# Optimization experiments

Hardware: AMD Instinct MI355X
Metric: run time of the kernel (lower is better)

Reference implementation:

```python
import jax, jax.numpy as jnp
import numpy as np

N_NODES = 50000
N_EDGES = 800000
IN_CH = 128
HID = 32
HEADS = 4
LATENT = 64
NEG_SLOPE = 0.2  # PyG GATConv default


def setup_inputs() -> dict:
    key = jax.random.key(0)
    ks = jax.random.split(key, 12)
    HC = HID * HEADS
    inp = {
        "x": jax.random.normal(ks[0], (N_NODES, IN_CH), dtype=jnp.float32),
        "edge_index": jax.random.randint(ks[1], (2, N_EDGES), 0, N_NODES, dtype=jnp.int64),
        # GATConv params
        "W_gat": jax.random.normal(ks[2], (IN_CH, HC), dtype=jnp.float32) / np.sqrt(IN_CH),
        "b_gat": jnp.zeros((HC,), dtype=jnp.float32),
        "att_src": jax.random.normal(ks[3], (HEADS, HID), dtype=jnp.float32) / np.sqrt(HID),
        "att_dst": jax.random.normal(ks[4], (HEADS, HID), dtype=jnp.float32) / np.sqrt(HID),
        # encoder / decoder / output linears
        "W_enc": jax.random.normal(ks[5], (HC, LATENT), dtype=jnp.float32) / np.sqrt(HC),
        "b_enc": jnp.zeros((LATENT,), dtype=jnp.float32),
        "W_dec": jax.random.normal(ks[6], (LATENT, HC), dtype=jnp.float32) / np.sqrt(LATENT),
        "b_dec": jnp.zeros((HC,), dtype=jnp.float32),
        "W_out": jax.random.normal(ks[7], (HC, IN_CH), dtype=jnp.float32) / np.sqrt(HC),
        "b_out": jnp.zeros((IN_CH,), dtype=jnp.float32),
    }
    return inp


def reference(x, edge_index, W_gat, b_gat, att_src, att_dst,
              W_enc, b_enc, W_dec, b_dec, W_out, b_out):
    N = x.shape[0]
    H, C = att_src.shape
    # PyG GATConv adds self-loops by default
    loops = jnp.arange(N, dtype=edge_index.dtype)
    src = jnp.concatenate([edge_index[0], loops])  # message sources (x_j)
    dst = jnp.concatenate([edge_index[1], loops])  # aggregation targets (x_i)

    h = (x @ W_gat).reshape(N, H, C)               # [N,H,C]
    a_src = jnp.einsum('nhc,hc->nh', h, att_src)   # [N,H]
    a_dst = jnp.einsum('nhc,hc->nh', h, att_dst)   # [N,H]

    e = jax.nn.leaky_relu(a_src[src] + a_dst[dst], NEG_SLOPE)  # [E,H]
    # segment softmax over destination nodes (numerically stable)
    e_max = jax.ops.segment_max(e, dst, num_segments=N)
    e_exp = jnp.exp(e - e_max[dst])
    denom = jax.ops.segment_sum(e_exp, dst, num_segments=N)
    alpha = e_exp / (denom[dst] + 1e-16)           # [E,H]

    msg = h[src] * alpha[:, :, None]               # [E,H,C]
    agg = jax.ops.segment_sum(msg, dst, num_segments=N)  # [N,H,C]
    gat_out = agg.reshape(N, H * C) + b_gat        # concat heads + bias

    x1 = jax.nn.elu(gat_out)
    encoded = x1 @ W_enc + b_enc
    decoded = encoded @ W_dec + b_dec
    x2 = jax.nn.elu(decoded)
    return x2 @ W_out + b_out
```

## Files before the change

kernel.cpp:

```cpp
#include <hip/hip_runtime.h>
#include <hip/hip_bf16.h>

#define N_NODES 50000
#define N_EDGES 800000
#define BM 64
#define NBUCK 196
#define CAP 8192
#define CHUNK 2048
#define NCHUNK ((N_EDGES + CHUNK - 1) / CHUNK)
#define SUBCAP 32
#define DCAP 5120
#define SWZ_BLOCKS 192
#define SWZ_G 32768
#define GBLK ((N_NODES + BM - 1) / BM)
#define SXP 136
#define SEP 72
#define SMEM_BYTES (64 * SXP * 2 + 64 * 132 * 4)

typedef _Float16 half4v __attribute__((ext_vector_type(4)));
typedef _Float16 half8 __attribute__((ext_vector_type(8)));
typedef float    float4v __attribute__((ext_vector_type(4)));

__device__ __forceinline__ float elu_f(float v) {
    return (v > 0.f) ? v : (__expf(v) - 1.f);
}

__device__ __forceinline__ unsigned f2bf2(float a, float b) {
    unsigned ua = __float_as_uint(a), ub = __float_as_uint(b);
    ua = (ua + 0x7FFFu + ((ua >> 16) & 1u)) >> 16;
    ub = (ub + 0x7FFFu + ((ub >> 16) & 1u)) >> 16;
    return ua | (ub << 16);
}
__device__ __forceinline__ float2 bf2f2(unsigned u) {
    float2 f;
    f.x = __uint_as_float(u << 16);
    f.y = __uint_as_float(u & 0xFFFF0000u);
    return f;
}

__global__ __launch_bounds__(256) void k_pre_bucket(const void* __restrict__ e_raw,
        const float* __restrict__ We, const float* __restrict__ Wd,
        const float* __restrict__ Wo, const float* __restrict__ Wg,
        _Float16* __restrict__ swz, uint2* __restrict__ ebuck2,
        int* __restrict__ cnt) {
    const int b = blockIdx.x;
    const int tid = threadIdx.x;
    if (b >= SWZ_BLOCKS) {
        __shared__ int lh[256];
        __shared__ int isl;
        const int c = b - SWZ_BLOCKS;
        const int base = c * CHUNK;
        const long long* e64 = (const long long*)e_raw;
        const int* e32 = (const int*)e_raw;
        if (tid == 0) {
            const unsigned* er = (const unsigned*)e_raw;
            int nz = 0;
            for (int j = 0; j < 64; j++) nz |= (er[2 * (base + j) + 1] != 0u);
            isl = nz ? 0 : 1;
        }
        lh[tid] = 0;
        __syncthreads();
        const int is64 = isl;
#pragma unroll 4
        for (int j = 0; j < CHUNK / 256; j++) {
            int e = base + j * 256 + tid;
            if (e < N_EDGES) {
                int sN, d;
                if (is64) { sN = (int)e64[e]; d = (int)e64[N_EDGES + e]; }
                else      { sN = e32[e];      d = e32[N_EDGES + e]; }
                int bb = d >> 8;
                int pos = atomicAdd(&lh[bb], 1);
                if (pos < SUBCAP) {
                    uint2 pr; pr.x = (unsigned)sN; pr.y = (unsigned)d;
                    ebuck2[((size_t)bb * NCHUNK + c) * SUBCAP + pos] = pr;
                }
            }
        }
        __syncthreads();
        int v = lh[tid]; if (v > SUBCAP) v = SUBCAP;
        cnt[c * 256 + tid] = v;
        return;
    }
    int t = b * 256 + tid;
    const float* W; int base, N;
    if (t < 8192)       { W = We; base = 0;     N = 64;  }
    else if (t < 16384) { W = Wd; base = 8192;  N = 128; }
    else if (t < 32768) { W = Wo; base = 16384; N = 128; }
    else                { W = Wg; base = SWZ_G; N = 128; }
    int loc = t - base;
    int nnt = N >> 4;
    int frag = loc >> 9, r = loc & 511, lane = r >> 3, j = r & 7;
    int kc = frag / nnt, nt = frag - kc * nnt;
    int k = kc * 32 + ((lane >> 4) << 3) + j;
    int n = nt * 16 + (lane & 15);
    swz[t] = (_Float16)W[k * N + n];
}

__global__ __launch_bounds__(256) void k_lin_bfill(
        const float* __restrict__ x, const _Float16* __restrict__ swz,
        const float* __restrict__ att_s, const float* __restrict__ att_d,
        unsigned* __restrict__ h_bf, float* __restrict__ a_src,
        float* __restrict__ a_dst,
        const uint2* __restrict__ ebuck2, const int* __restrict__ cnt,
        int2* __restrict__ nodeoff, int* __restrict__ csr_src) {
    __shared__ __align__(16) char smem[SMEM_BYTES];
    const int tid = threadIdx.x;

    if (blockIdx.x < NBUCK) {
        uint2* dense = (uint2*)smem;
        int*   coff  = (int*)(smem + 40960);
        int*   sc    = (int*)(smem + 42528);
        int*   lh    = (int*)(smem + 43552);
        int*   lexc  = (int*)(smem + 44576);
        int*   lcur  = (int*)(smem + 45600);
        const int bkt = blockIdx.x;
        const int lo = bkt * CAP;
        const int n0 = bkt << 8;

        int v0 = cnt[tid * 256 + bkt];
        sc[tid] = v0;
        __syncthreads();
        for (int o = 1; o < 256; o <<= 1) {
            int u = (tid >= o) ? sc[tid - o] : 0;
            __syncthreads();
            sc[tid] += u;
            __syncthreads();
        }
        coff[tid] = sc[tid] - v0;
        int total0 = sc[255];
        __syncthreads();
        int c2 = tid + 256;
        int v1 = (c2 < NCHUNK) ? cnt[c2 * 256 + bkt] : 0;
        sc[tid] = v1;
        __syncthreads();
        for (int o = 1; o < 256; o <<= 1) {
            int u = (tid >= o) ? sc[tid - o] : 0;
            __syncthreads();
            sc[tid] += u;
            __syncthreads();
        }
        if (c2 < NCHUNK) coff[c2] = total0 + sc[tid] - v1;
        int cntb = total0 + sc[255];
        if (cntb > DCAP) cntb = DCAP;
        if (tid == 0) coff[NCHUNK] = cntb;
        __syncthreads();

        {
            int cg = tid >> 3, j = tid & 7;
            for (int c = cg; c < NCHUNK; c += 32) {
                int off = coff[c];
                int n = coff[c + 1] - off;
                const uint2* src = &ebuck2[((size_t)bkt * NCHUNK + c) * SUBCAP];
                for (int e = j; e < n; e += 8)
                    if (off + e < DCAP) dense[off + e] = src[e];
            }
        }
        __syncthreads();

        lh[tid] = 0;
        lcur[tid] = 0;
        __syncthreads();
        for (int i = tid; i < cntb; i += 256)
            atomicAdd(&lh[dense[i].y & 255], 1);
        __syncthreads();

        int v = lh[tid];
        int p = (v + 7) & ~7;
        lexc[tid] = p;
        __syncthreads();
        for (int o = 1; o < 256; o <<= 1) {
            int u = (tid >= o) ? lexc[tid - o] : 0;
            __syncthreads();
            lexc[tid] += u;
            __syncthreads();
        }
        {
            int s = lexc[tid] - p;
            lexc[tid] = s;
            int node = n0 + tid;
            if (node < N_NODES) {
                int2 no;
                no.x = lo + s;
                int maxlen = CAP - s; if (maxlen < 0) maxlen = 0;
                no.y = p <= maxlen ? p : (maxlen & ~7);
                nodeoff[node] = no;
            }
        }
        __syncthreads();

        for (int i = tid; i < cntb; i += 256) {
            uint2 pr = dense[i];
            int li = (int)(pr.y & 255);
            int pos = atomicAdd(&lcur[li], 1);
            int dst = lexc[li] + pos;
            if (dst < CAP) csr_src[lo + dst] = (int)pr.x;
        }
        {
            int base2 = lexc[tid];
            for (int j = v; j < p && base2 + j < CAP; j++)
                csr_src[lo + base2 + j] = -1;
        }
        return;
    }

    _Float16* sx = (_Float16*)smem;
    float*    sh = (float*)(smem + 64 * SXP * 2);
    const int m0 = (blockIdx.x - NBUCK) * 64;

#pragma unroll
    for (int i = 0; i < 8; i++) {
        int idx = tid + i * 256;
        int r = idx >> 5, c4 = idx & 31;
        int row = m0 + r; if (row >= N_NODES) row = N_NODES - 1;
        float4 v = ((const float4*)(x + (size_t)row * 128))[c4];
        half4v h;
        h[0] = (_Float16)v.x; h[1] = (_Float16)v.y;
        h[2] = (_Float16)v.z; h[3] = (_Float16)v.w;
        *(half4v*)&sx[r * SXP + c4 * 4] = h;
    }
    __syncthreads();

    const int wave = tid >> 6, lane = tid & 63;
    const int lm = lane & 15, lq = lane >> 4;
    const int wrow = wave * 16;

    {
        float4v acc[8];
#pragma unroll
        for (int nt = 0; nt < 8; nt++) acc[nt] = (float4v){0.f, 0.f, 0.f, 0.f};
#pragma unroll
        for (int kc = 0; kc < 4; kc++) {
            half8 a = *(const half8*)&sx[(wrow + lm) * SXP + kc * 32 + lq * 8];
#pragma unroll
            for (int nt = 0; nt < 8; nt++) {
                half8 b = *(const half8*)&swz[SWZ_G + (kc * 8 + nt) * 512 + lane * 8];
                acc[nt] = __builtin_amdgcn_mfma_f32_16x16x32_f16(a, b, acc[nt], 0, 0, 0);
            }
        }
#pragma unroll
        for (int nt = 0; nt < 8; nt++)
#pragma unroll
            for (int r = 0; r < 4; r++)
                sh[(wrow + lq * 4 + r) * 132 + nt * 16 + lm] = acc[nt][r];
    }
    __syncthreads();

    const int c0 = (tid & 31) * 4;
    const int r0 = (tid >> 5) * 8;
    float4 as4 = *(const float4*)&att_s[c0];
    float4 ad4 = *(const float4*)&att_d[c0];
    const int head = c0 >> 5;

#pragma unroll
    for (int r = 0; r < 8; r++) {
        int row = m0 + r0 + r;
        bool ok = row < N_NODES;
        float4 hv = *(const float4*)&sh[(r0 + r) * 132 + c0];
        if (ok) {
            uint2 p;
            p.x = f2bf2(hv.x, hv.y);
            p.y = f2bf2(hv.z, hv.w);
            *(uint2*)&h_bf[(size_t)row * 64 + (c0 >> 1)] = p;
        }
        float vs = hv.x * as4.x + hv.y * as4.y + hv.z * as4.z + hv.w * as4.w;
        float vd = hv.x * ad4.x + hv.y * ad4.y + hv.z * ad4.z + hv.w * ad4.w;
#pragma unroll
        for (int o = 4; o >= 1; o >>= 1) {
            vs += __shfl_down(vs, o, 8);
            vd += __shfl_down(vd, o, 8);
        }
        if (ok && (tid & 7) == 0) {
            a_src[row * 4 + head] = vs;
            a_dst[row * 4 + head] = vd;
        }
    }
}

__global__ __launch_bounds__(256) void k_gather(const int2* __restrict__ nodeoff,
        const int* __restrict__ csr_src, const float* __restrict__ a_src,
        const float* __restrict__ a_dst, const unsigned* __restrict__ h_bf,
        const float* __restrict__ b_gat, _Float16* __restrict__ x1) {
    int d = blockIdx.x * 4 + (threadIdx.x >> 6);
    if (d >= N_NODES) return;
    const int lane = threadIdx.x & 63;
    const int eg = lane >> 4;
    const int lc = lane & 15;
    const int hd = lc >> 2;
    const uint4* hb = (const uint4*)h_bf;
    int2 nd = nodeoff[d];
    const int lo = nd.x, hi = nd.x + nd.y;

    const float adh = a_dst[(unsigned)(d * 4 + hd)];

    float den = 0.f;
    float c0 = 0.f, c1 = 0.f, c2 = 0.f, c3 = 0.f;
    float c4 = 0.f, c5 = 0.f, c6 = 0.f, c7 = 0.f;

    if (eg == 0) {
        float t = a_src[(unsigned)(d * 4 + hd)] + adh;
        t = t > 0.f ? t : 0.2f * t;
        float es = __expf(t);
        den = es;
        uint4 u = hb[(unsigned)d * 16 + lc];
        float2 p0 = bf2f2(u.x), p1 = bf2f2(u.y), p2 = bf2f2(u.z), p3 = bf2f2(u.w);
        c0 = p0.x * es; c1 = p0.y * es; c2 = p1.x * es; c3 = p1.y * es;
        c4 = p2.x * es; c5 = p2.y * es; c6 = p3.x * es; c7 = p3.y * es;
    }

    for (int base = lo; base < hi; base += 8) {
        int2 sv = *(const int2*)&csr_src[base + eg * 2];
        int sA = sv.x, sB = sv.y;
        unsigned gA = (unsigned)(sA < 0 ? d : sA);
        unsigned gB = (unsigned)(sB < 0 ? d : sB);
        uint4 uA = hb[gA * 16 + lc];
        uint4 uB = hb[gB * 16 + lc];
        float aA = a_src[gA * 4 + hd];
        float aB = a_src[gB * 4 + hd];

        float tA = aA + adh; tA = tA > 0.f ? tA : 0.2f * tA;
        float tB = aB + adh; tB = tB > 0.f ? tB : 0.2f * tB;
        float eA = sA < 0 ? 0.f : __expf(tA);
        float eB = sB < 0 ? 0.f : __expf(tB);
        den += eA + eB;

        float2 p0, p1, p2, p3;
        p0 = bf2f2(uA.x); p1 = bf2f2(uA.y); p2 = bf2f2(uA.z); p3 = bf2f2(uA.w);
        c0 = fmaf(p0.x, eA, c0); c1 = fmaf(p0.y, eA, c1);
        c2 = fmaf(p1.x, eA, c2); c3 = fmaf(p1.y, eA, c3);
        c4 = fmaf(p2.x, eA, c4); c5 = fmaf(p2.y, eA, c5);
        c6 = fmaf(p3.x, eA, c6); c7 = fmaf(p3.y, eA, c7);
        p0 = bf2f2(uB.x); p1 = bf2f2(uB.y); p2 = bf2f2(uB.z); p3 = bf2f2(uB.w);
        c0 = fmaf(p0.x, eB, c0); c1 = fmaf(p0.y, eB, c1);
        c2 = fmaf(p1.x, eB, c2); c3 = fmaf(p1.y, eB, c3);
        c4 = fmaf(p2.x, eB, c4); c5 = fmaf(p2.y, eB, c5);
        c6 = fmaf(p3.x, eB, c6); c7 = fmaf(p3.y, eB, c7);
    }

    den += __shfl_xor(den, 16);
    c0 += __shfl_xor(c0, 16); c1 += __shfl_xor(c1, 16);
    c2 += __shfl_xor(c2, 16); c3 += __shfl_xor(c3, 16);
    c4 += __shfl_xor(c4, 16); c5 += __shfl_xor(c5, 16);
    c6 += __shfl_xor(c6, 16); c7 += __shfl_xor(c7, 16);
    den += __shfl_xor(den, 32);
    c0 += __shfl_xor(c0, 32); c1 += __shfl_xor(c1, 32);
    c2 += __shfl_xor(c2, 32); c3 += __shfl_xor(c3, 32);
    c4 += __shfl_xor(c4, 32); c5 += __shfl_xor(c5, 32);
    c6 += __shfl_xor(c6, 32); c7 += __shfl_xor(c7, 32);

    if (lane < 16) {
        float inv = 1.f / (den + 1e-16f);
        float4 bg0 = ((const float4*)b_gat)[lc * 2];
        float4 bg1 = ((const float4*)b_gat)[lc * 2 + 1];
        half8 hv;
        hv[0] = (_Float16)elu_f(fmaf(c0, inv, bg0.x));
        hv[1] = (_Float16)elu_f(fmaf(c1, inv, bg0.y));
        hv[2] = (_Float16)elu_f(fmaf(c2, inv, bg0.z));
        hv[3] = (_Float16)elu_f(fmaf(c3, inv, bg0.w));
        hv[4] = (_Float16)elu_f(fmaf(c4, inv, bg1.x));
        hv[5] = (_Float16)elu_f(fmaf(c5, inv, bg1.y));
        hv[6] = (_Float16)elu_f(fmaf(c6, inv, bg1.z));
        hv[7] = (_Float16)elu_f(fmaf(c7, inv, bg1.w));
        *(half8*)&x1[(size_t)d * 128 + lc * 8] = hv;
    }
}

__global__ __launch_bounds__(256) void k_mlp(const _Float16* __restrict__ x1,
        const _Float16* __restrict__ swz, const float* __restrict__ b_enc,
        const float* __restrict__ b_dec, const float* __restrict__ b_out,
        float* __restrict__ out) {
    __shared__ _Float16 sx[64 * SXP];
    __shared__ _Float16 se[4 * 16 * SEP];
    const int tid = threadIdx.x;
    const int m0 = blockIdx.x * 64;

#pragma unroll
    for (int i = 0; i < 4; i++) {
        int idx = tid + i * 256;
        int r = idx >> 4, c = idx & 15;
        int row = m0 + r; if (row >= N_NODES) row = N_NODES - 1;
        uint4 v = ((const uint4*)(x1 + (size_t)row * 128))[c];
        *(uint4*)&sx[r * SXP + c * 8] = v;
    }
    __syncthreads();

    const int wave = tid >> 6, lane = tid & 63;
    const int lm = lane & 15, lq = lane >> 4;
    const int wrow = wave * 16;
    _Float16* eslab = &se[wave * 16 * SEP];

    {
        float4v acc[4];
#pragma unroll
        for (int nt = 0; nt < 4; nt++) acc[nt] = (float4v){0.f, 0.f, 0.f, 0.f};
#pragma unroll
        for (int kc = 0; kc < 4; kc++) {
            half8 a = *(const half8*)&sx[(wrow + lm) * SXP + kc * 32 + lq * 8];
#pragma unroll
            for (int nt = 0; nt < 4; nt++) {
                half8 b = *(const half8*)&swz[(kc * 4 + nt) * 512 + lane * 8];
                acc[nt] = __builtin_amdgcn_mfma_f32_16x16x32_f16(a, b, acc[nt], 0, 0, 0);
            }
        }
#pragma unroll
        for (int nt = 0; nt < 4; nt++) {
            float be = b_enc[nt * 16 + lm];
#pragma unroll
            for (int r = 0; r < 4; r++)
                eslab[(lq * 4 + r) * SEP + nt * 16 + lm] = (_Float16)(acc[nt][r] + be);
        }
    }

    {
        float4v acc[8];
#pragma unroll
        for (int nt = 0; nt < 8; nt++) acc[nt] = (float4v){0.f, 0.f, 0.f, 0.f};
#pragma unroll
        for (int kc = 0; kc < 2; kc++) {
            half8 a = *(const half8*)&eslab[lm * SEP + kc * 32 + lq * 8];
#pragma unroll
            for (int nt = 0; nt < 8; nt++) {
                half8 b = *(const half8*)&swz[8192 + (kc * 8 + nt) * 512 + lane * 8];
                acc[nt] = __builtin_amdgcn_mfma_f32_16x16x32_f16(a, b, acc[nt], 0, 0, 0);
            }
        }
#pragma unroll
        for (int nt = 0; nt < 8; nt++) {
            float bd = b_dec[nt * 16 + lm];
#pragma unroll
            for (int r = 0; r < 4; r++)
                sx[(wrow + lq * 4 + r) * SXP + nt * 16 + lm] =
                    (_Float16)elu_f(acc[nt][r] + bd);
        }
    }

    {
        float4v acc[8];
#pragma unroll
        for (int nt = 0; nt < 8; nt++) acc[nt] = (float4v){0.f, 0.f, 0.f, 0.f};
#pragma unroll
        for (int kc = 0; kc < 4; kc++) {
            half8 a = *(const half8*)&sx[(wrow + lm) * SXP + kc * 32 + lq * 8];
#pragma unroll
            for (int nt = 0; nt < 8; nt++) {
                half8 b = *(const half8*)&swz[16384 + (kc * 8 + nt) * 512 + lane * 8];
                acc[nt] = __builtin_amdgcn_mfma_f32_16x16x32_f16(a, b, acc[nt], 0, 0, 0);
            }
        }
#pragma unroll
        for (int nt = 0; nt < 8; nt++) {
            float bo = b_out[nt * 16 + lm];
#pragma unroll
            for (int r = 0; r < 4; r++) {
                int row = m0 + wrow + lq * 4 + r;
                if (row < N_NODES)
                    out[(size_t)row * 128 + nt * 16 + lm] = acc[nt][r] + bo;
            }
        }
    }
}

extern "C" void kernel_launch(void* const* d_in, const int* in_sizes, int n_in,
                              void* d_out, int out_size, void* d_ws, size_t ws_size,
                              hipStream_t stream) {
    const float* x       = (const float*)d_in[0];
    const void*  e_raw   = d_in[1];
    const float* W_gat   = (const float*)d_in[2];
    const float* b_gat   = (const float*)d_in[3];
    const float* att_src = (const float*)d_in[4];
    const float* att_dst = (const float*)d_in[5];
    const float* W_enc   = (const float*)d_in[6];
    const float* b_enc   = (const float*)d_in[7];
    const float* W_dec   = (const float*)d_in[8];
    const float* b_dec   = (const float*)d_in[9];
    const float* W_out   = (const float*)d_in[10];
    const float* b_out   = (const float*)d_in[11];
    float* out = (float*)d_out;

    float* ws      = (float*)d_ws;
    unsigned* h_bf = (unsigned*)ws;
    float* a_src   = ws + 6400000;
    float* a_dst   = a_src + 200000;
    float* agg     = a_dst + 200000;
    uint2* ebuck2  = (uint2*)agg;
    _Float16* x1   = (_Float16*)agg;
    int*   csr_src = (int*)(agg + 6400000);
    int*   cnt     = csr_src + NBUCK * CAP;
    int2*  nodeoff = (int2*)(cnt + NCHUNK * 256);
    _Float16* swz  = (_Float16*)(((uintptr_t)(nodeoff + 50000) + 15) & ~(uintptr_t)15);

    k_pre_bucket<<<SWZ_BLOCKS + NCHUNK, 256, 0, stream>>>(
        e_raw, W_enc, W_dec, W_out, W_gat, swz, ebuck2, cnt);

    k_lin_bfill<<<NBUCK + GBLK, 256, 0, stream>>>(
        x, swz, att_src, att_dst, h_bf, a_src, a_dst,
        ebuck2, cnt, nodeoff, csr_src);

    k_gather<<<(N_NODES + 3) / 4, 256, 0, stream>>>(
        nodeoff, csr_src, a_src, a_dst, h_bf, b_gat, x1);

    k_mlp<<<GBLK, 256, 0, stream>>>(x1, swz, b_enc, b_dec, b_out, out);
}
```

Measured before the change: 175.3 us.

## Fuse GAT gather with MLP chain in one 1024-thread block kernel

Merges the edge gather/softmax-aggregation kernel and the three-layer MFMA MLP kernel into one kernel. Each 1024-thread block gathers 64 destination nodes (4 per wave) straight into shared memory, then 16 waves split the MLP output columns. This removes the fp16 x1 round trip through global memory and one kernel launch. In exchange it adds block-wide barriers between stages, and the large blocks may lower occupancy and leave waves idle when node degrees are uneven.

```diff
diff --git a/kernel.cpp b/kernel.cpp
--- a/kernel.cpp
+++ b/kernel.cpp
@@ -276,184 +276,178 @@
     }
 }
 
-__global__ __launch_bounds__(256) void k_gather(const int2* __restrict__ nodeoff,
-        const int* __restrict__ csr_src, const float* __restrict__ a_src,
-        const float* __restrict__ a_dst, const unsigned* __restrict__ h_bf,
-        const float* __restrict__ b_gat, _Float16* __restrict__ x1) {
-    int d = blockIdx.x * 4 + (threadIdx.x >> 6);
-    if (d >= N_NODES) return;
-    const int lane = threadIdx.x & 63;
+__global__ __launch_bounds__(1024) void k_gather_mlp(
+        const int2* __restrict__ nodeoff, const int* __restrict__ csr_src,
+        const float* __restrict__ a_src, const float* __restrict__ a_dst,
+        const unsigned* __restrict__ h_bf, const float* __restrict__ b_gat,
+        const _Float16* __restrict__ swz, const float* __restrict__ b_enc,
+        const float* __restrict__ b_dec, const float* __restrict__ b_out,
+        float* __restrict__ out) {
+    __shared__ _Float16 sx[64 * SXP];
+    __shared__ _Float16 se[64 * SEP];
+    const int tid = threadIdx.x;
+    const int wave = tid >> 6, lane = tid & 63;
+    const int m0 = blockIdx.x * 64;
     const int eg = lane >> 4;
     const int lc = lane & 15;
     const int hd = lc >> 2;
     const uint4* hb = (const uint4*)h_bf;
-    int2 nd = nodeoff[d];
-    const int lo = nd.x, hi = nd.x + nd.y;
-
-    const float adh = a_dst[(unsigned)(d * 4 + hd)];
-
-    float den = 0.f;
-    float c0 = 0.f, c1 = 0.f, c2 = 0.f, c3 = 0.f;
-    float c4 = 0.f, c5 = 0.f, c6 = 0.f, c7 = 0.f;
-
-    if (eg == 0) {
-        float t = a_src[(unsigned)(d * 4 + hd)] + adh;
-        t = t > 0.f ? t : 0.2f * t;
-        float es = __expf(t);
-        den = es;
-        uint4 u = hb[(unsigned)d * 16 + lc];
-        float2 p0 = bf2f2(u.x), p1 = bf2f2(u.y), p2 = bf2f2(u.z), p3 = bf2f2(u.w);
-        c0 = p0.x * es; c1 = p0.y * es; c2 = p1.x * es; c3 = p1.y * es;
-        c4 = p2.x * es; c5 = p2.y * es; c6 = p3.x * es; c7 = p3.y * es;
-    }
-
-    for (int base = lo; base < hi; base += 8) {
-        int2 sv = *(const int2*)&csr_src[base + eg * 2];
-        int sA = sv.x, sB = sv.y;
-        unsigned gA = (unsigned)(sA < 0 ? d : sA);
-        unsigned gB = (unsigned)(sB < 0 ? d : sB);
-        uint4 uA = hb[gA * 16 + lc];
-        uint4 uB = hb[gB * 16 + lc];
-        float aA = a_src[gA * 4 + hd];
-        float aB = a_src[gB * 4 + hd];
-
-        float tA = aA + adh; tA = tA > 0.f ? tA : 0.2f * tA;
-        float tB = aB + adh; tB = tB > 0.f ? tB : 0.2f * tB;
-        float eA = sA < 0 ? 0.f : __expf(tA);
-        float eB = sB < 0 ? 0.f : __expf(tB);
-        den += eA + eB;
-
-        float2 p0, p1, p2, p3;
-        p0 = bf2f2(uA.x); p1 = bf2f2(uA.y); p2 = bf2f2(uA.z); p3 = bf2f2(uA.w);
-        c0 = fmaf(p0.x, eA, c0); c1 = fmaf(p0.y, eA, c1);
-        c2 = fmaf(p1.x, eA, c2); c3 = fmaf(p1.y, eA, c3);
-        c4 = fmaf(p2.x, eA, c4); c5 = fmaf(p2.y, eA, c5);
-        c6 = fmaf(p3.x, eA, c6); c7 = fmaf(p3.y, eA, c7);
-        p0 = bf2f2(uB.x); p1 = bf2f2(uB.y); p2 = bf2f2(uB.z); p3 = bf2f2(uB.w);
-        c0 = fmaf(p0.x, eB, c0); c1 = fmaf(p0.y, eB, c1);
-        c2 = fmaf(p1.x, eB, c2); c3 = fmaf(p1.y, eB, c3);
-        c4 = fmaf(p2.x, eB, c4); c5 = fmaf(p2.y, eB, c5);
-        c6 = fmaf(p3.x, eB, c6); c7 = fmaf(p3.y, eB, c7);
-    }
-
-    den += __shfl_xor(den, 16);
-    c0 += __shfl_xor(c0, 16); c1 += __shfl_xor(c1, 16);
-    c2 += __shfl_xor(c2, 16); c3 += __shfl_xor(c3, 16);
-    c4 += __shfl_xor(c4, 16); c5 += __shfl_xor(c5, 16);
-    c6 += __shfl_xor(c6, 16); c7 += __shfl_xor(c7, 16);
-    den += __shfl_xor(den, 32);
-    c0 += __shfl_xor(c0, 32); c1 += __shfl_xor(c1, 32);
-    c2 += __shfl_xor(c2, 32); c3 += __shfl_xor(c3, 32);
-    c4 += __shfl_xor(c4, 32); c5 += __shfl_xor(c5, 32);
-    c6 += __shfl_xor(c6, 32); c7 += __shfl_xor(c7, 32);
-
-    if (lane < 16) {
-        float inv = 1.f / (den + 1e-16f);
-        float4 bg0 = ((const float4*)b_gat)[lc * 2];
-        float4 bg1 = ((const float4*)b_gat)[lc * 2 + 1];
-        half8 hv;
-        hv[0] = (_Float16)elu_f(fmaf(c0, inv, bg0.x));
-        hv[1] = (_Float16)elu_f(fmaf(c1, inv, bg0.y));
-        hv[2] = (_Float16)elu_f(fmaf(c2, inv, bg0.z));
-        hv[3] = (_Float16)elu_f(fmaf(c3, inv, bg0.w));
-        hv[4] = (_Float16)elu_f(fmaf(c4, inv, bg1.x));
-        hv[5] = (_Float16)elu_f(fmaf(c5, inv, bg1.y));
-        hv[6] = (_Float16)elu_f(fmaf(c6, inv, bg1.z));
-        hv[7] = (_Float16)elu_f(fmaf(c7, inv, bg1.w));
-        *(half8*)&x1[(size_t)d * 128 + lc * 8] = hv;
-    }
-}
-
-__global__ __launch_bounds__(256) void k_mlp(const _Float16* __restrict__ x1,
-        const _Float16* __restrict__ swz, const float* __restrict__ b_enc,
-        const float* __restrict__ b_dec, const float* __restrict__ b_out,
-        float* __restrict__ out) {
-    __shared__ _Float16 sx[64 * SXP];
-    __shared__ _Float16 se[4 * 16 * SEP];
-    const int tid = threadIdx.x;
-    const int m0 = blockIdx.x * 64;
-
-#pragma unroll
-    for (int i = 0; i < 4; i++) {
-        int idx = tid + i * 256;
-        int r = idx >> 4, c = idx & 15;
-        int row = m0 + r; if (row >= N_NODES) row = N_NODES - 1;
-        uint4 v = ((const uint4*)(x1 + (size_t)row * 128))[c];
-        *(uint4*)&sx[r * SXP + c * 8] = v;
+    const float4 bg0 = ((const float4*)b_gat)[lc * 2];
+    const float4 bg1 = ((const float4*)b_gat)[lc * 2 + 1];
+
+    for (int k = 0; k < 4; k++) {
+        const int r = wave * 4 + k;
+        const int d = m0 + r;
+        if (d < N_NODES) {
+            int2 nd = nodeoff[d];
+            const int lo = nd.x, hi = nd.x + nd.y;
+            const float adh = a_dst[(unsigned)(d * 4 + hd)];
+
+            float den = 0.f;
+            float c0 = 0.f, c1 = 0.f, c2 = 0.f, c3 = 0.f;
+            float c4 = 0.f, c5 = 0.f, c6 = 0.f, c7 = 0.f;
+
+            if (eg == 0) {
+                float t = a_src[(unsigned)(d * 4 + hd)] + adh;
+                t = t > 0.f ? t : 0.2f * t;
+                float es = __expf(t);
+                den = es;
+                uint4 u = hb[(unsigned)d * 16 + lc];
+                float2 p0 = bf2f2(u.x), p1 = bf2f2(u.y),
+                       p2 = bf2f2(u.z), p3 = bf2f2(u.w);
+                c0 = p0.x * es; c1 = p0.y * es; c2 = p1.x * es; c3 = p1.y * es;
+                c4 = p2.x * es; c5 = p2.y * es; c6 = p3.x * es; c7 = p3.y * es;
+            }
+
+            for (int base = lo; base < hi; base += 8) {
+                int2 sv = *(const int2*)&csr_src[base + eg * 2];
+                int sA = sv.x, sB = sv.y;
+                unsigned gA = (unsigned)(sA < 0 ? d : sA);
+                unsigned gB = (unsigned)(sB < 0 ? d : sB);
+                uint4 uA = hb[gA * 16 + lc];
+                uint4 uB = hb[gB * 16 + lc];
+                float aA = a_src[gA * 4 + hd];
+                float aB = a_src[gB * 4 + hd];
+
+                float tA = aA + adh; tA = tA > 0.f ? tA : 0.2f * tA;
+                float tB = aB + adh; tB = tB > 0.f ? tB : 0.2f * tB;
+                float eA = sA < 0 ? 0.f : __expf(tA);
+                float eB = sB < 0 ? 0.f : __expf(tB);
+                den += eA + eB;
+
+                float2 p0, p1, p2, p3;
+                p0 = bf2f2(uA.x); p1 = bf2f2(uA.y);
+                p2 = bf2f2(uA.z); p3 = bf2f2(uA.w);
+                c0 = fmaf(p0.x, eA, c0); c1 = fmaf(p0.y, eA, c1);
+                c2 = fmaf(p1.x, eA, c2); c3 = fmaf(p1.y, eA, c3);
+                c4 = fmaf(p2.x, eA, c4); c5 = fmaf(p2.y, eA, c5);
+                c6 = fmaf(p3.x, eA, c6); c7 = fmaf(p3.y, eA, c7);
+                p0 = bf2f2(uB.x); p1 = bf2f2(uB.y);
+                p2 = bf2f2(uB.z); p3 = bf2f2(uB.w);
+                c0 = fmaf(p0.x, eB, c0); c1 = fmaf(p0.y, eB, c1);
+                c2 = fmaf(p1.x, eB, c2); c3 = fmaf(p1.y, eB, c3);
+                c4 = fmaf(p2.x, eB, c4); c5 = fmaf(p2.y, eB, c5);
+                c6 = fmaf(p3.x, eB, c6); c7 = fmaf(p3.y, eB, c7);
+            }
+
+            den += __shfl_xor(den, 16);
+            c0 += __shfl_xor(c0, 16); c1 += __shfl_xor(c1, 16);
+            c2 += __shfl_xor(c2, 16); c3 += __shfl_xor(c3, 16);
+            c4 += __shfl_xor(c4, 16); c5 += __shfl_xor(c5, 16);
+            c6 += __shfl_xor(c6, 16); c7 += __shfl_xor(c7, 16);
+            den += __shfl_xor(den, 32);
+            c0 += __shfl_xor(c0, 32); c1 += __shfl_xor(c1, 32);
+            c2 += __shfl_xor(c2, 32); c3 += __shfl_xor(c3, 32);
+            c4 += __shfl_xor(c4, 32); c5 += __shfl_xor(c5, 32);
+            c6 += __shfl_xor(c6, 32); c7 += __shfl_xor(c7, 32);
+
+            if (eg == 0) {
+                float inv = 1.f / (den + 1e-16f);
+                half8 hv;
+                hv[0] = (_Float16)elu_f(fmaf(c0, inv, bg0.x));
+                hv[1] = (_Float16)elu_f(fmaf(c1, inv, bg0.y));
+                hv[2] = (_Float16)elu_f(fmaf(c2, inv, bg0.z));
+                hv[3] = (_Float16)elu_f(fmaf(c3, inv, bg0.w));
+                hv[4] = (_Float16)elu_f(fmaf(c4, inv, bg1.x));
+                hv[5] = (_Float16)elu_f(fmaf(c5, inv, bg1.y));
+                hv[6] = (_Float16)elu_f(fmaf(c6, inv, bg1.z));
+                hv[7] = (_Float16)elu_f(fmaf(c7, inv, bg1.w));
+                *(half8*)&sx[r * SXP + lc * 8] = hv;
+            }
+        } else if (eg == 0) {
+            *(half8*)&sx[r * SXP + lc * 8] = (half8){0, 0, 0, 0, 0, 0, 0, 0};
+        }
     }
     __syncthreads();
 
-    const int wave = tid >> 6, lane = tid & 63;
     const int lm = lane & 15, lq = lane >> 4;
-    const int wrow = wave * 16;
-    _Float16* eslab = &se[wave * 16 * SEP];
+    const int wr = wave >> 2, wn = wave & 3;
+    const int wrow = wr * 16;
 
     {
-        float4v acc[4];
-#pragma unroll
-        for (int nt = 0; nt < 4; nt++) acc[nt] = (float4v){0.f, 0.f, 0.f, 0.f};
+        float4v acc = (float4v){0.f, 0.f, 0.f, 0.f};
 #pragma unroll
         for (int kc = 0; kc < 4; kc++) {
             half8 a = *(const half8*)&sx[(wrow + lm) * SXP + kc * 32 + lq * 8];
-#pragma unroll
-            for (int nt = 0; nt < 4; nt++) {
-                half8 b = *(const half8*)&swz[(kc * 4 + nt) * 512 + lane * 8];
-                acc[nt] = __builtin_amdgcn_mfma_f32_16x16x32_f16(a, b, acc[nt], 0, 0, 0);
-            }
-        }
-#pragma unroll
-        for (int nt = 0; nt < 4; nt++) {
-            float be = b_enc[nt * 16 + lm];
-#pragma unroll
-            for (int r = 0; r < 4; r++)
-                eslab[(lq * 4 + r) * SEP + nt * 16 + lm] = (_Float16)(acc[nt][r] + be);
-        }
-    }
+            half8 b = *(const half8*)&swz[(kc * 4 + wn) * 512 + lane * 8];
+            acc = __builtin_amdgcn_mfma_f32_16x16x32_f16(a, b, acc, 0, 0, 0);
+        }
+        float be = b_enc[wn * 16 + lm];
+#pragma unroll
+        for (int r = 0; r < 4; r++)
+            se[(wrow + lq * 4 + r) * SEP + wn * 16 + lm] = (_Float16)(acc[r] + be);
+    }
+    __syncthreads();
 
     {
-        float4v acc[8];
-#pragma unroll
-        for (int nt = 0; nt < 8; nt++) acc[nt] = (float4v){0.f, 0.f, 0.f, 0.f};
+        float4v acc[2];
+        acc[0] = (float4v){0.f, 0.f, 0.f, 0.f};
+        acc[1] = (float4v){0.f, 0.f, 0.f, 0.f};
 #pragma unroll
         for (int kc = 0; kc < 2; kc++) {
-            half8 a = *(const half8*)&eslab[lm * SEP + kc * 32 + lq * 8];
-#pragma unroll
-            for (int nt = 0; nt < 8; nt++) {
+            half8 a = *(const half8*)&se[(wrow + lm) * SEP + kc * 32 + lq * 8];
+#pragma unroll
+            for (int t = 0; t < 2; t++) {
+                int nt = wn * 2 + t;
                 half8 b = *(const half8*)&swz[8192 + (kc * 8 + nt) * 512 + lane * 8];
-                acc[nt] = __builtin_amdgcn_mfma_f32_16x16x32_f16(a, b, acc[nt], 0, 0, 0);
-            }
-        }
-#pragma unroll
-        for (int nt = 0; nt < 8; nt++) {
+                acc[t] = __builtin_amdgcn_mfma_f32_16x16x32_f16(a, b, acc[t], 0, 0, 0);
+            }
+        }
+#pragma unroll
+        for (int t = 0; t < 2; t++) {
+            int nt = wn * 2 + t;
             float bd = b_dec[nt * 16 + lm];
 #pragma unroll
             for (int r = 0; r < 4; r++)
                 sx[(wrow + lq * 4 + r) * SXP + nt * 16 + lm] =
-                    (_Float16)elu_f(acc[nt][r] + bd);
-        }
-    }
+                    (_Float16)elu_f(acc[t][r] + bd);
+        }
+    }
+    __syncthreads();
 
     {
-        float4v acc[8];
-#pragma unroll
-        for (int nt = 0; nt < 8; nt++) acc[nt] = (float4v){0.f, 0.f, 0.f, 0.f};
+        float4v acc[2];
+        acc[0] = (float4v){0.f, 0.f, 0.f, 0.f};
+        acc[1] = (float4v){0.f, 0.f, 0.f, 0.f};
 #pragma unroll
         for (int kc = 0; kc < 4; kc++) {
             half8 a = *(const half8*)&sx[(wrow + lm) * SXP + kc * 32 + lq * 8];
 #pragma unroll
-            for (int nt = 0; nt < 8; nt++) {
+            for (int t = 0; t < 2; t++) {
+                int nt = wn * 2 + t;
                 half8 b = *(const half8*)&swz[16384 + (kc * 8 + nt) * 512 + lane * 8];
-                acc[nt] = __builtin_amdgcn_mfma_f32_16x16x32_f16(a, b, acc[nt], 0, 0, 0);
-            }
-        }
-#pragma unroll
-        for (int nt = 0; nt < 8; nt++) {
+                acc[t] = __builtin_amdgcn_mfma_f32_16x16x32_f16(a, b, acc[t], 0, 0, 0);
+            }
+        }
+#pragma unroll
+        for (int t = 0; t < 2; t++) {
+            int nt = wn * 2 + t;
             float bo = b_out[nt * 16 + lm];
 #pragma unroll
             for (int r = 0; r < 4; r++) {
                 int row = m0 + wrow + lq * 4 + r;
                 if (row < N_NODES)
-                    out[(size_t)row * 128 + nt * 16 + lm] = acc[nt][r] + bo;
+                    out[(size_t)row * 128 + nt * 16 + lm] = acc[t][r] + bo;
             }
         }
     }
@@ -482,7 +476,6 @@
     float* a_dst   = a_src + 200000;
     float* agg     = a_dst + 200000;
     uint2* ebuck2  = (uint2*)agg;
-    _Float16* x1   = (_Float16*)agg;
     int*   csr_src = (int*)(agg + 6400000);
     int*   cnt     = csr_src + NBUCK * CAP;
     int2*  nodeoff = (int2*)(cnt + NCHUNK * 256);
@@ -495,8 +488,7 @@
         x, swz, att_src, att_dst, h_bf, a_src, a_dst,
         ebuck2, cnt, nodeoff, csr_src);
 
-    k_gather<<<(N_NODES + 3) / 4, 256, 0, stream>>>(
-        nodeoff, csr_src, a_src, a_dst, h_bf, b_gat, x1);
-
-    k_mlp<<<GBLK, 256, 0, stream>>>(x1, swz, b_enc, b_dec, b_out, out);
-}
+    k_gather_mlp<<<GBLK, 1024, 0, stream>>>(
+        nodeoff, csr_src, a_src, a_dst, h_bf, b_gat, swz,
+        b_enc, b_dec, b_out, out);
+}
```

New measurement: 176.0 us. No clear change (+0.4%).

## Split h into per-head planes and gather each head in a separate block set

Applied to the files above, without the earlier changes.

The bf16 projected features are stored as four head-major planes instead of interleaved rows. The gather kernel launches four times as many blocks, one set per head. Each wavefront processes 32 edges per iteration for a single head, using 4 lanes per 64-byte row. The aim is a smaller working set per head plane for better L2 hit rate and more parallelism on low-degree nodes. In exchange, each edge index and a_src value is re-read four times, and padded slots are now guarded with bounds checks.

```diff
diff --git a/kernel.cpp b/kernel.cpp
--- a/kernel.cpp
+++ b/kernel.cpp
@@ -16,6 +16,9 @@
 #define SXP 136
 #define SEP 72
 #define SMEM_BYTES (64 * SXP * 2 + 64 * 132 * 4)
+#define NQ 4
+#define NBPQ ((N_NODES + 3) / 4)
+#define HPLANE 800000
 
 typedef _Float16 half4v __attribute__((ext_vector_type(4)));
 typedef _Float16 half8 __attribute__((ext_vector_type(8)));
@@ -250,6 +253,8 @@
     float4 as4 = *(const float4*)&att_s[c0];
     float4 ad4 = *(const float4*)&att_d[c0];
     const int head = c0 >> 5;
+    const int pl = c0 >> 5;
+    const int ci = (c0 & 31) >> 1;
 
 #pragma unroll
     for (int r = 0; r < 8; r++) {
@@ -260,7 +265,7 @@
             uint2 p;
             p.x = f2bf2(hv.x, hv.y);
             p.y = f2bf2(hv.z, hv.w);
-            *(uint2*)&h_bf[(size_t)row * 64 + (c0 >> 1)] = p;
+            *(uint2*)&h_bf[(size_t)pl * HPLANE + (size_t)row * 16 + ci] = p;
         }
         float vs = hv.x * as4.x + hv.y * as4.y + hv.z * as4.z + hv.w * as4.w;
         float vd = hv.x * ad4.x + hv.y * ad4.y + hv.z * ad4.z + hv.w * ad4.w;
@@ -280,42 +285,46 @@
         const int* __restrict__ csr_src, const float* __restrict__ a_src,
         const float* __restrict__ a_dst, const unsigned* __restrict__ h_bf,
         const float* __restrict__ b_gat, _Float16* __restrict__ x1) {
-    int d = blockIdx.x * 4 + (threadIdx.x >> 6);
+    const int q  = blockIdx.x / NBPQ;
+    const int nb = blockIdx.x - q * NBPQ;
+    int d = nb * 4 + (threadIdx.x >> 6);
     if (d >= N_NODES) return;
     const int lane = threadIdx.x & 63;
-    const int eg = lane >> 4;
-    const int lc = lane & 15;
-    const int hd = lc >> 2;
-    const uint4* hb = (const uint4*)h_bf;
+    const int eg  = lane >> 2;
+    const int lc2 = lane & 3;
+    const uint4* hb = (const uint4*)(h_bf + (size_t)q * HPLANE);
     int2 nd = nodeoff[d];
     const int lo = nd.x, hi = nd.x + nd.y;
 
-    const float adh = a_dst[(unsigned)(d * 4 + hd)];
+    const float adh = a_dst[(unsigned)(d * 4 + q)];
 
     float den = 0.f;
     float c0 = 0.f, c1 = 0.f, c2 = 0.f, c3 = 0.f;
     float c4 = 0.f, c5 = 0.f, c6 = 0.f, c7 = 0.f;
 
     if (eg == 0) {
-        float t = a_src[(unsigned)(d * 4 + hd)] + adh;
+        float t = a_src[(unsigned)(d * 4 + q)] + adh;
         t = t > 0.f ? t : 0.2f * t;
         float es = __expf(t);
         den = es;
-        uint4 u = hb[(unsigned)d * 16 + lc];
+        uint4 u = hb[(unsigned)d * 4 + lc2];
         float2 p0 = bf2f2(u.x), p1 = bf2f2(u.y), p2 = bf2f2(u.z), p3 = bf2f2(u.w);
         c0 = p0.x * es; c1 = p0.y * es; c2 = p1.x * es; c3 = p1.y * es;
         c4 = p2.x * es; c5 = p2.y * es; c6 = p3.x * es; c7 = p3.y * es;
     }
 
-    for (int base = lo; base < hi; base += 8) {
-        int2 sv = *(const int2*)&csr_src[base + eg * 2];
-        int sA = sv.x, sB = sv.y;
+    for (int base = lo; base < hi; base += 32) {
+        int i0 = base + eg * 2;
+        int2 sv = *(const int2*)&csr_src[i0];
+        bool ok = i0 < hi;
+        int sA = ok ? sv.x : -1;
+        int sB = ok ? sv.y : -1;
         unsigned gA = (unsigned)(sA < 0 ? d : sA);
         unsigned gB = (unsigned)(sB < 0 ? d : sB);
-        uint4 uA = hb[gA * 16 + lc];
-        uint4 uB = hb[gB * 16 + lc];
-        float aA = a_src[gA * 4 + hd];
-        float aB = a_src[gB * 4 + hd];
+        uint4 uA = hb[gA * 4 + lc2];
+        uint4 uB = hb[gB * 4 + lc2];
+        float aA = a_src[gA * 4 + q];
+        float aB = a_src[gB * 4 + q];
 
         float tA = aA + adh; tA = tA > 0.f ? tA : 0.2f * tA;
         float tB = aB + adh; tB = tB > 0.f ? tB : 0.2f * tB;
@@ -336,21 +345,19 @@
         c6 = fmaf(p3.x, eB, c6); c7 = fmaf(p3.y, eB, c7);
     }
 
-    den += __shfl_xor(den, 16);
-    c0 += __shfl_xor(c0, 16); c1 += __shfl_xor(c1, 16);
-    c2 += __shfl_xor(c2, 16); c3 += __shfl_xor(c3, 16);
-    c4 += __shfl_xor(c4, 16); c5 += __shfl_xor(c5, 16);
-    c6 += __shfl_xor(c6, 16); c7 += __shfl_xor(c7, 16);
-    den += __shfl_xor(den, 32);
-    c0 += __shfl_xor(c0, 32); c1 += __shfl_xor(c1, 32);
-    c2 += __shfl_xor(c2, 32); c3 += __shfl_xor(c3, 32);
-    c4 += __shfl_xor(c4, 32); c5 += __shfl_xor(c5, 32);
-    c6 += __shfl_xor(c6, 32); c7 += __shfl_xor(c7, 32);
-
-    if (lane < 16) {
+#pragma unroll
+    for (int o = 4; o <= 32; o <<= 1) {
+        den += __shfl_xor(den, o);
+        c0 += __shfl_xor(c0, o); c1 += __shfl_xor(c1, o);
+        c2 += __shfl_xor(c2, o); c3 += __shfl_xor(c3, o);
+        c4 += __shfl_xor(c4, o); c5 += __shfl_xor(c5, o);
+        c6 += __shfl_xor(c6, o); c7 += __shfl_xor(c7, o);
+    }
+
+    if (lane < 4) {
         float inv = 1.f / (den + 1e-16f);
-        float4 bg0 = ((const float4*)b_gat)[lc * 2];
-        float4 bg1 = ((const float4*)b_gat)[lc * 2 + 1];
+        float4 bg0 = ((const float4*)b_gat)[q * 8 + lc2 * 2];
+        float4 bg1 = ((const float4*)b_gat)[q * 8 + lc2 * 2 + 1];
         half8 hv;
         hv[0] = (_Float16)elu_f(fmaf(c0, inv, bg0.x));
         hv[1] = (_Float16)elu_f(fmaf(c1, inv, bg0.y));
@@ -360,7 +367,7 @@
         hv[5] = (_Float16)elu_f(fmaf(c5, inv, bg1.y));
         hv[6] = (_Float16)elu_f(fmaf(c6, inv, bg1.z));
         hv[7] = (_Float16)elu_f(fmaf(c7, inv, bg1.w));
-        *(half8*)&x1[(size_t)d * 128 + lc * 8] = hv;
+        *(half8*)&x1[(size_t)d * 128 + q * 32 + lc2 * 8] = hv;
     }
 }
 
@@ -495,7 +502,7 @@
         x, swz, att_src, att_dst, h_bf, a_src, a_dst,
         ebuck2, cnt, nodeoff, csr_src);
 
-    k_gather<<<(N_NODES + 3) / 4, 256, 0, stream>>>(
+    k_gather<<<NQ * NBPQ, 256, 0, stream>>>(
         nodeoff, csr_src, a_src, a_dst, h_bf, b_gat, x1);
 
     k_mlp<<<GBLK, 256, 0, stream>>>(x1, swz, b_enc, b_dec, b_out, out);
```

Result: slower. 221.1 us (+26.1%).
